# Performance work log

Hardware: AMD Instinct MI355X
Metric: run time of the kernel (lower is better)

## Reference

```python
import jax, jax.numpy as jnp
import numpy as np

B, TQ, TK, D, V = 16, 64, 512, 256, 32000


def setup_inputs() -> dict:
    key = jax.random.key(0)
    k = jax.random.split(key, 8)
    return {
        "domainslots": jax.random.normal(k[0], (B, TQ, D), jnp.float32),
        "out_states": jax.random.normal(k[1], (B, TQ, D), jnp.float32),
        "context": jax.random.normal(k[2], (B, TK, D), jnp.float32),
        "context_plain": jax.random.randint(k[3], (B, TK), 0, V, jnp.int64 if jax.config.jax_enable_x64 else jnp.int32),
        "W_state": jax.random.normal(k[4], (D, V), jnp.float32) * 0.02,
        "b_state": jnp.zeros((V,), jnp.float32),
        "W_gen": jax.random.normal(k[5], (3 * D, 1), jnp.float32) * 0.02,
        "b_gen": jnp.zeros((1,), jnp.float32),
    }


def reference(domainslots, out_states, context, context_plain, W_state, b_state, W_gen, b_gen):
    d = out_states.shape[-1]
    # pointer attention: softmax(Q K^T / sqrt(d)) over context  -> [B, TQ, TK]
    scores = jnp.einsum("bqd,bkd->bqk", out_states, context) / jnp.sqrt(jnp.asarray(d, out_states.dtype))
    pointer_attn = jax.nn.softmax(scores, axis=-1)

    # generation distribution over vocab  -> [B, TQ, V]
    p_state_vocab = jax.nn.softmax(out_states @ W_state + b_state, axis=-1)

    # copy distribution: scatter-add attention mass onto source token ids
    b_idx = jnp.arange(B)[:, None, None]           # [B,1,1]
    q_idx = jnp.arange(TQ)[None, :, None]          # [1,TQ,1]
    v_idx = context_plain[:, None, :]              # [B,1,TK] broadcast over TQ
    p_state_ptr = jnp.zeros((B, TQ, V), p_state_vocab.dtype).at[b_idx, q_idx, v_idx].add(pointer_attn)

    # attention-weighted context vector  -> [B, TQ, D]
    context_vec = jnp.einsum("bqk,bkd->bqd", pointer_attn, context)

    # generation gate  -> [B, TQ, 1]
    p_gen_vec = jnp.concatenate([out_states, context_vec, domainslots], axis=-1)
    p_state_gen = jax.nn.sigmoid(p_gen_vec @ W_gen + b_gen)

    p_state_out = p_state_gen * p_state_vocab + (1.0 - p_state_gen) * p_state_ptr
    return jnp.log(p_state_out)
```

## Files before the change

kernel.cpp:

```cpp
#include <hip/hip_runtime.h>
#include <math.h>

typedef short short8 __attribute__((ext_vector_type(8)));
typedef float f32x4 __attribute__((ext_vector_type(4)));

#define B_ 16
#define TQ_ 64
#define TK_ 512
#define D_ 256
#define V_ 32000
#define M_ (B_ * TQ_)

__device__ __forceinline__ unsigned short f2bf(float x) {
    unsigned int u = __float_as_uint(x);
    unsigned int r = (u + 0x7fffu + ((u >> 16) & 1u)) >> 16;
    return (unsigned short)r;
}

__device__ __forceinline__ void gload_lds16(const void* g, void* l) {
    __builtin_amdgcn_global_load_lds(
        (const __attribute__((address_space(1))) void*)g,
        (__attribute__((address_space(3))) void*)l, 16, 0, 0);
}

__global__ __launch_bounds__(256) void dedup_kernel(
    const int* __restrict__ cp, int* __restrict__ nexta, int* __restrict__ leader)
{
    __shared__ __align__(16) int c[TK_];
    const int b = blockIdx.x, tid = threadIdx.x;
    c[tid] = cp[b * TK_ + tid];
    c[tid + 256] = cp[b * TK_ + 256 + tid];
    __syncthreads();
    for (int k = tid; k < TK_; k += 256) {
        const int v = c[k];
        int fm = 1024, nx = 1024;
#pragma unroll 8
        for (int j0 = 0; j0 < TK_; j0 += 4) {
            const int4 q = *(const int4*)&c[j0];
            if (q.x == v) { fm = min(fm, j0);     if (j0     > k) nx = min(nx, j0);     }
            if (q.y == v) { fm = min(fm, j0 + 1); if (j0 + 1 > k) nx = min(nx, j0 + 1); }
            if (q.z == v) { fm = min(fm, j0 + 2); if (j0 + 2 > k) nx = min(nx, j0 + 2); }
            if (q.w == v) { fm = min(fm, j0 + 3); if (j0 + 3 > k) nx = min(nx, j0 + 3); }
        }
        nexta[b * TK_ + k] = (nx < 1024) ? nx : -1;
        leader[b * TK_ + k] = (fm == k) ? 1 : 0;
    }
}

__global__ __launch_bounds__(256) void conv_a_kernel(
    const float* __restrict__ A, unsigned short* __restrict__ Ab)
{
    const int i = (blockIdx.x * 256 + threadIdx.x) * 4;
    const float4 v = *(const float4*)&A[i];
    ushort4 o;
    o.x = f2bf(v.x); o.y = f2bf(v.y); o.z = f2bf(v.z); o.w = f2bf(v.w);
    *(ushort4*)&Ab[i] = o;
}

__global__ __launch_bounds__(256) void conv_w_kernel(
    const float* __restrict__ W, unsigned short* __restrict__ Wt)
{
    __shared__ float tile[64][65];
    const int tid = threadIdx.x;
    const int k0 = (blockIdx.x & 3) * 64;
    const int n0 = (blockIdx.x >> 2) * 64;
#pragma unroll
    for (int i = 0; i < 16; i++) {
        const int r = i * 4 + (tid >> 6), cc = tid & 63;
        tile[r][cc] = W[(k0 + r) * V_ + n0 + cc];
    }
    __syncthreads();
#pragma unroll
    for (int i = 0; i < 4; i++) {
        const int nl = i * 16 + (tid >> 4);
        const int kq = (tid & 15) * 4;
        ushort4 o;
        o.x = f2bf(tile[kq + 0][nl]);
        o.y = f2bf(tile[kq + 1][nl]);
        o.z = f2bf(tile[kq + 2][nl]);
        o.w = f2bf(tile[kq + 3][nl]);
        *(ushort4*)&Wt[(n0 + nl) * D_ + k0 + kq] = o;
    }
}

__global__ __launch_bounds__(256) void conv_c_kernel(
    const float* __restrict__ ctx, unsigned short* __restrict__ Cb,
    unsigned short* __restrict__ Ct)
{
    __shared__ float tile[64][65];
    const int tid = threadIdx.x;
    const int b = blockIdx.x >> 5;
    const int r5 = blockIdx.x & 31;
    const int k0 = (r5 >> 2) * 64;
    const int d0 = (r5 & 3) * 64;
#pragma unroll
    for (int i = 0; i < 16; i++) {
        const int r = i * 4 + (tid >> 6), cc = tid & 63;
        const float v = ctx[((b * TK_) + k0 + r) * D_ + d0 + cc];
        tile[r][cc] = v;
        Cb[((b * TK_) + k0 + r) * D_ + d0 + cc] = f2bf(v);
    }
    __syncthreads();
#pragma unroll
    for (int i = 0; i < 4; i++) {
        const int dl = i * 16 + (tid >> 4);
        const int kq = (tid & 15) * 4;
        ushort4 o;
        o.x = f2bf(tile[kq + 0][dl]);
        o.y = f2bf(tile[kq + 1][dl]);
        o.z = f2bf(tile[kq + 2][dl]);
        o.w = f2bf(tile[kq + 3][dl]);
        *(ushort4*)&Ct[((b * D_) + d0 + dl) * TK_ + k0 + kq] = o;
    }
}

template <int LDA, int LDB, int KTOT>
__global__ __launch_bounds__(256) void gemm_small(
    const unsigned short* __restrict__ A,
    const unsigned short* __restrict__ Bt,
    float* __restrict__ C, int ldc, int nchunks, int btrows, float scale)
{
    __shared__ short Al[64][72];
    __shared__ short Bl[128][72];
    const int tid = threadIdx.x;
    const int b = blockIdx.x / nchunks;
    const int n0 = (blockIdx.x % nchunks) * 128;
    A += (size_t)b * 64 * LDA;
    Bt += (size_t)b * btrows * LDB;
    C += (size_t)b * 64 * ldc;

    const int wid = tid >> 6;
    const int lane = tid & 63;
    const int wm = wid & 1, wn = wid >> 1;
    const int quad = lane >> 4, l15 = lane & 15;

    f32x4 acc[2][4];
#pragma unroll
    for (int i = 0; i < 2; i++)
#pragma unroll
        for (int j = 0; j < 4; j++) acc[i][j] = f32x4{0.f, 0.f, 0.f, 0.f};

    for (int k0 = 0; k0 < KTOT; k0 += 64) {
        __syncthreads();
#pragma unroll
        for (int i = 0; i < 2; i++) {
            const int c = tid + i * 256;
            const int r = c >> 3, kc = (c & 7) * 8;
            *(uint4*)&Al[r][kc] = *(const uint4*)&A[r * LDA + k0 + kc];
        }
#pragma unroll
        for (int i = 0; i < 4; i++) {
            const int c = tid + i * 256;
            const int r = c >> 3, kc = (c & 7) * 8;
            *(uint4*)&Bl[r][kc] = *(const uint4*)&Bt[(n0 + r) * LDB + k0 + kc];
        }
        __syncthreads();
#pragma unroll
        for (int ks = 0; ks < 64; ks += 32) {
            short8 af[2], bf[4];
#pragma unroll
            for (int mt = 0; mt < 2; mt++)
                af[mt] = *(const short8*)&Al[wm * 32 + mt * 16 + l15][ks + quad * 8];
#pragma unroll
            for (int nt = 0; nt < 4; nt++)
                bf[nt] = *(const short8*)&Bl[wn * 64 + nt * 16 + l15][ks + quad * 8];
#pragma unroll
            for (int mt = 0; mt < 2; mt++)
#pragma unroll
                for (int nt = 0; nt < 4; nt++)
                    acc[mt][nt] = __builtin_amdgcn_mfma_f32_16x16x32_bf16(
                        af[mt], bf[nt], acc[mt][nt], 0, 0, 0);
        }
    }
#pragma unroll
    for (int mt = 0; mt < 2; mt++)
#pragma unroll
        for (int nt = 0; nt < 4; nt++)
#pragma unroll
            for (int r = 0; r < 4; r++) {
                const int rl = wm * 32 + mt * 16 + quad * 4 + r;
                const int col = n0 + wn * 64 + nt * 16 + l15;
                C[rl * ldc + col] = acc[mt][nt][r] * scale;
            }
}

__global__ __launch_bounds__(256) void softmax_kernel(
    float* __restrict__ S, unsigned short* __restrict__ Pb)
{
    const int w = threadIdx.x >> 6, lane = threadIdx.x & 63;
    const int row = blockIdx.x * 4 + w;
    float v[8], m = -1e30f;
#pragma unroll
    for (int j = 0; j < 8; j++) { v[j] = S[row * TK_ + lane + 64 * j]; m = fmaxf(m, v[j]); }
#pragma unroll
    for (int off = 32; off; off >>= 1) m = fmaxf(m, __shfl_xor(m, off));
    float s = 0.f;
#pragma unroll
    for (int j = 0; j < 8; j++) { v[j] = __expf(v[j] - m); s += v[j]; }
#pragma unroll
    for (int off = 32; off; off >>= 1) s += __shfl_xor(s, off);
    const float inv = 1.0f / s;
#pragma unroll
    for (int j = 0; j < 8; j++) {
        const float p = v[j] * inv;
        S[row * TK_ + lane + 64 * j] = p;
        Pb[row * TK_ + lane + 64 * j] = f2bf(p);
    }
}

__global__ __launch_bounds__(256) void pgen_kernel(
    const float* __restrict__ os, const float* __restrict__ cv,
    const float* __restrict__ dm, const float* __restrict__ W_gen,
    const float* __restrict__ b_gen, float* __restrict__ pg)
{
    const int w = threadIdx.x >> 6, lane = threadIdx.x & 63;
    const int row = blockIdx.x * 4 + w;
    const int d4 = lane * 4;
    const float4 o4 = *(const float4*)&os[row * D_ + d4];
    const float4 c4 = *(const float4*)&cv[row * D_ + d4];
    const float4 m4 = *(const float4*)&dm[row * D_ + d4];
    const float4 w0 = *(const float4*)&W_gen[d4];
    const float4 w1 = *(const float4*)&W_gen[D_ + d4];
    const float4 w2 = *(const float4*)&W_gen[2 * D_ + d4];
    float p = o4.x * w0.x + o4.y * w0.y + o4.z * w0.z + o4.w * w0.w
            + c4.x * w1.x + c4.y * w1.y + c4.z * w1.z + c4.w * w1.w
            + m4.x * w2.x + m4.y * w2.y + m4.z * w2.z + m4.w * w2.w;
#pragma unroll
    for (int off = 32; off; off >>= 1) p += __shfl_xor(p, off);
    if (lane == 0) pg[row] = 1.0f / (1.0f + __expf(-(p + b_gen[0])));
}

__global__ __launch_bounds__(256) void gemm_vocab_fused(
    const unsigned short* __restrict__ A,
    const unsigned short* __restrict__ Bt,
    const float* __restrict__ b_state,
    float* __restrict__ Z,
    float* __restrict__ out)
{
    __shared__ short Al[128][64];
    __shared__ short Bl[128][64];
    __shared__ float bst[128];

    const int tid = threadIdx.x;
    const int bx = blockIdx.x;
    const int m0 = (bx & 7) * 128;
    const int n0 = (bx >> 3) * 128;

    if (tid < 128) bst[tid] = b_state[n0 + tid];

    const int wid = tid >> 6, lane = tid & 63;
    const int wm = wid & 1, wn = wid >> 1;
    const int quad = lane >> 4, l15 = lane & 15;
    const int srow = lane >> 3;
    const int scol = (lane & 7) * 8;

    f32x4 acc[4][4];
#pragma unroll
    for (int i = 0; i < 4; i++)
#pragma unroll
        for (int j = 0; j < 4; j++) acc[i][j] = f32x4{0.f, 0.f, 0.f, 0.f};

    for (int k0 = 0; k0 < D_; k0 += 64) {
        __syncthreads();
#pragma unroll
        for (int j = 0; j < 4; j++) {
            const int c = j * 4 + wid;
            const int r = c * 8 + srow;
            gload_lds16(&A[(size_t)(m0 + r) * D_ + k0 + scol], &Al[c * 8][0]);
        }
#pragma unroll
        for (int j = 0; j < 4; j++) {
            const int c = j * 4 + wid;
            const int r = c * 8 + srow;
            gload_lds16(&Bt[(size_t)(n0 + r) * D_ + k0 + scol], &Bl[c * 8][0]);
        }
        __syncthreads();
#pragma unroll
        for (int ks = 0; ks < 64; ks += 32) {
            short8 af[4], bf[4];
#pragma unroll
            for (int mt = 0; mt < 4; mt++)
                af[mt] = *(const short8*)&Al[wm * 64 + mt * 16 + l15][ks + quad * 8];
#pragma unroll
            for (int nt = 0; nt < 4; nt++)
                bf[nt] = *(const short8*)&Bl[wn * 64 + nt * 16 + l15][ks + quad * 8];
#pragma unroll
            for (int mt = 0; mt < 4; mt++)
#pragma unroll
                for (int nt = 0; nt < 4; nt++)
                    acc[mt][nt] = __builtin_amdgcn_mfma_f32_16x16x32_bf16(
                        af[mt], bf[nt], acc[mt][nt], 0, 0, 0);
        }
    }

#pragma unroll
    for (int mt = 0; mt < 4; mt++) {
        float rs[4] = {0.f, 0.f, 0.f, 0.f};
#pragma unroll
        for (int nt = 0; nt < 4; nt++) {
            const float bcol = bst[wn * 64 + nt * 16 + l15];
#pragma unroll
            for (int r = 0; r < 4; r++) {
                const int row = wm * 64 + mt * 16 + quad * 4 + r;
                const int col = wn * 64 + nt * 16 + l15;
                const float v = acc[mt][nt][r] + bcol;
                out[(size_t)(m0 + row) * V_ + n0 + col] = v;
                rs[r] += __expf(v);
            }
        }
#pragma unroll
        for (int r = 0; r < 4; r++) {
            float v = rs[r];
            v += __shfl_xor(v, 1);
            v += __shfl_xor(v, 2);
            v += __shfl_xor(v, 4);
            v += __shfl_xor(v, 8);
            if (l15 == 0)
                atomicAdd(&Z[m0 + wm * 64 + mt * 16 + quad * 4 + r], v);
        }
    }
}

__global__ __launch_bounds__(256) void rowconst_kernel(
    const float* __restrict__ pg, const float* __restrict__ Z, float* __restrict__ rc)
{
    const int r = blockIdx.x * 256 + threadIdx.x;
    rc[r] = logf(pg[r]) - logf(Z[r]);
}

__global__ __launch_bounds__(256) void epilogue_kernel(
    const float* __restrict__ rc, float* __restrict__ out)
{
    const int row = blockIdx.x;
    const float r = rc[row];
    float4* p = (float4*)(out + (size_t)row * V_);
    for (int i = threadIdx.x; i < V_ / 4; i += 256) {
        float4 v = p[i];
        v.x += r; v.y += r; v.z += r; v.w += r;
        p[i] = v;
    }
}

__global__ __launch_bounds__(256) void fixup_kernel(
    const int* __restrict__ cp, const int* __restrict__ nexta,
    const int* __restrict__ leader, const float* __restrict__ attn,
    const float* __restrict__ pg, float* __restrict__ out)
{
    const int t = blockIdx.x * 256 + threadIdx.x;
    const int row = t >> 9, k = t & 511;
    const int b = row >> 6;
    if (!leader[b * TK_ + k]) return;
    float a = attn[row * TK_ + k];
    int j = nexta[b * TK_ + k];
    while (j >= 0) { a += attn[row * TK_ + j]; j = nexta[b * TK_ + j]; }
    const float val = (1.0f - pg[row]) * a;
    const int v = cp[b * TK_ + k];
    const size_t idx = (size_t)row * V_ + v;
    out[idx] = logf(expf(out[idx]) + val);
}

extern "C" void kernel_launch(void* const* d_in, const int* in_sizes, int n_in,
                              void* d_out, int out_size, void* d_ws, size_t ws_size,
                              hipStream_t stream)
{
    const float* domainslots = (const float*)d_in[0];
    const float* out_states  = (const float*)d_in[1];
    const float* context     = (const float*)d_in[2];
    const int*   cp          = (const int*)d_in[3];
    const float* W_state     = (const float*)d_in[4];
    const float* b_state     = (const float*)d_in[5];
    const float* W_gen       = (const float*)d_in[6];
    const float* b_gen       = (const float*)d_in[7];
    float* out = (float*)d_out;
    char* ws = (char*)d_ws;

    float* Z      = (float*)(ws);
    float* pg     = (float*)(ws + 4096);
    float* rc     = (float*)(ws + 8192);
    float* S      = (float*)(ws + 12288);
    int* nexta    = (int*)(ws + 2109440);
    int* leader   = (int*)(ws + 2142208);
    unsigned short* Ab = (unsigned short*)(ws + 2174976);
    unsigned short* Wt = (unsigned short*)(ws + 2699264);
    unsigned short* Cb = (unsigned short*)(ws + 19083264);
    unsigned short* Ct = (unsigned short*)(ws + 23277568);
    unsigned short* Pb = (unsigned short*)(ws + 27471872);
    float* cv     = (float*)(ws + 28520448);

    hipMemsetAsync(Z, 0, M_ * sizeof(float), stream);
    dedup_kernel<<<B_, 256, 0, stream>>>(cp, nexta, leader);
    conv_a_kernel<<<(M_ * D_) / 1024, 256, 0, stream>>>(out_states, Ab);
    conv_w_kernel<<<(D_ / 64) * (V_ / 64), 256, 0, stream>>>(W_state, Wt);
    conv_c_kernel<<<B_ * 32, 256, 0, stream>>>(context, Cb, Ct);

    gemm_small<D_, D_, D_><<<B_ * 4, 256, 0, stream>>>(Ab, Cb, S, TK_, 4, TK_, 0.0625f);
    softmax_kernel<<<M_ / 4, 256, 0, stream>>>(S, Pb);
    gemm_small<TK_, TK_, TK_><<<B_ * 2, 256, 0, stream>>>(Pb, Ct, cv, D_, 2, D_, 1.0f);
    pgen_kernel<<<M_ / 4, 256, 0, stream>>>(out_states, cv, domainslots, W_gen, b_gen, pg);

    gemm_vocab_fused<<<(M_ / 128) * (V_ / 128), 256, 0, stream>>>(Ab, Wt, b_state, Z, out);
    rowconst_kernel<<<M_ / 256, 256, 0, stream>>>(pg, Z, rc);
    epilogue_kernel<<<M_, 256, 0, stream>>>(rc, out);
    fixup_kernel<<<(M_ * TK_) / 256, 256, 0, stream>>>(cp, nexta, leader, S, pg, out);
}
```

Measured before the change: 349.6 us.

## Recompute vocab GEMM twice to drop the logits read-modify-write epilogue

Splits the fused vocab GEMM into two passes. The first computes only the per-row exp-sums Z with no output store. The second recomputes the GEMM and writes the final log-probabilities directly, folding in log(pg) - log(Z) per row. This replaces the separate rowconst and epilogue kernels, removing a full read and write of the 131 MB output in exchange for doubling the bf16 GEMM work. Block indices are also swizzled across the grid so that concurrently running blocks share tiles differently for cache reuse.

```diff
diff --git a/kernel.cpp b/kernel.cpp
--- a/kernel.cpp
+++ b/kernel.cpp
@@ -230,21 +230,20 @@
     if (lane == 0) pg[row] = 1.0f / (1.0f + __expf(-(p + b_gen[0])));
 }
 
-__global__ __launch_bounds__(256) void gemm_vocab_fused(
+__global__ __launch_bounds__(256) void gemm_vocab_z(
     const unsigned short* __restrict__ A,
     const unsigned short* __restrict__ Bt,
     const float* __restrict__ b_state,
-    float* __restrict__ Z,
-    float* __restrict__ out)
+    float* __restrict__ Z)
 {
     __shared__ short Al[128][64];
     __shared__ short Bl[128][64];
     __shared__ float bst[128];
 
     const int tid = threadIdx.x;
-    const int bx = blockIdx.x;
-    const int m0 = (bx & 7) * 128;
-    const int n0 = (bx >> 3) * 128;
+    const int swz = (blockIdx.x & 7) * 250 + (blockIdx.x >> 3);
+    const int m0 = (swz & 7) * 128;
+    const int n0 = (swz >> 3) * 128;
 
     if (tid < 128) bst[tid] = b_state[n0 + tid];
 
@@ -300,13 +299,8 @@
         for (int nt = 0; nt < 4; nt++) {
             const float bcol = bst[wn * 64 + nt * 16 + l15];
 #pragma unroll
-            for (int r = 0; r < 4; r++) {
-                const int row = wm * 64 + mt * 16 + quad * 4 + r;
-                const int col = wn * 64 + nt * 16 + l15;
-                const float v = acc[mt][nt][r] + bcol;
-                out[(size_t)(m0 + row) * V_ + n0 + col] = v;
-                rs[r] += __expf(v);
-            }
+            for (int r = 0; r < 4; r++)
+                rs[r] += __expf(acc[mt][nt][r] + bcol);
         }
 #pragma unroll
         for (int r = 0; r < 4; r++) {
@@ -321,23 +315,86 @@
     }
 }
 
-__global__ __launch_bounds__(256) void rowconst_kernel(
-    const float* __restrict__ pg, const float* __restrict__ Z, float* __restrict__ rc)
-{
-    const int r = blockIdx.x * 256 + threadIdx.x;
-    rc[r] = logf(pg[r]) - logf(Z[r]);
-}
-
-__global__ __launch_bounds__(256) void epilogue_kernel(
-    const float* __restrict__ rc, float* __restrict__ out)
-{
-    const int row = blockIdx.x;
-    const float r = rc[row];
-    float4* p = (float4*)(out + (size_t)row * V_);
-    for (int i = threadIdx.x; i < V_ / 4; i += 256) {
-        float4 v = p[i];
-        v.x += r; v.y += r; v.z += r; v.w += r;
-        p[i] = v;
+__global__ __launch_bounds__(256) void gemm_vocab_out(
+    const unsigned short* __restrict__ A,
+    const unsigned short* __restrict__ Bt,
+    const float* __restrict__ b_state,
+    const float* __restrict__ pg,
+    const float* __restrict__ Z,
+    float* __restrict__ out)
+{
+    __shared__ short Al[128][64];
+    __shared__ short Bl[128][64];
+    __shared__ float bst[128];
+    __shared__ float rcs[128];
+
+    const int tid = threadIdx.x;
+    const int swz = (blockIdx.x & 7) * 250 + (blockIdx.x >> 3);
+    const int m0 = (swz & 7) * 128;
+    const int n0 = (swz >> 3) * 128;
+
+    if (tid < 128) {
+        bst[tid] = b_state[n0 + tid];
+        rcs[tid] = logf(pg[m0 + tid]) - logf(Z[m0 + tid]);
+    }
+
+    const int wid = tid >> 6, lane = tid & 63;
+    const int wm = wid & 1, wn = wid >> 1;
+    const int quad = lane >> 4, l15 = lane & 15;
+    const int srow = lane >> 3;
+    const int scol = (lane & 7) * 8;
+
+    f32x4 acc[4][4];
+#pragma unroll
+    for (int i = 0; i < 4; i++)
+#pragma unroll
+        for (int j = 0; j < 4; j++) acc[i][j] = f32x4{0.f, 0.f, 0.f, 0.f};
+
+    for (int k0 = 0; k0 < D_; k0 += 64) {
+        __syncthreads();
+#pragma unroll
+        for (int j = 0; j < 4; j++) {
+            const int c = j * 4 + wid;
+            const int r = c * 8 + srow;
+            gload_lds16(&A[(size_t)(m0 + r) * D_ + k0 + scol], &Al[c * 8][0]);
+        }
+#pragma unroll
+        for (int j = 0; j < 4; j++) {
+            const int c = j * 4 + wid;
+            const int r = c * 8 + srow;
+            gload_lds16(&Bt[(size_t)(n0 + r) * D_ + k0 + scol], &Bl[c * 8][0]);
+        }
+        __syncthreads();
+#pragma unroll
+        for (int ks = 0; ks < 64; ks += 32) {
+            short8 af[4], bf[4];
+#pragma unroll
+            for (int mt = 0; mt < 4; mt++)
+                af[mt] = *(const short8*)&Al[wm * 64 + mt * 16 + l15][ks + quad * 8];
+#pragma unroll
+            for (int nt = 0; nt < 4; nt++)
+                bf[nt] = *(const short8*)&Bl[wn * 64 + nt * 16 + l15][ks + quad * 8];
+#pragma unroll
+            for (int mt = 0; mt < 4; mt++)
+#pragma unroll
+                for (int nt = 0; nt < 4; nt++)
+                    acc[mt][nt] = __builtin_amdgcn_mfma_f32_16x16x32_bf16(
+                        af[mt], bf[nt], acc[mt][nt], 0, 0, 0);
+        }
+    }
+
+#pragma unroll
+    for (int mt = 0; mt < 4; mt++) {
+#pragma unroll
+        for (int nt = 0; nt < 4; nt++) {
+            const float bcol = bst[wn * 64 + nt * 16 + l15];
+#pragma unroll
+            for (int r = 0; r < 4; r++) {
+                const int row = wm * 64 + mt * 16 + quad * 4 + r;
+                const int col = wn * 64 + nt * 16 + l15;
+                out[(size_t)(m0 + row) * V_ + n0 + col] = acc[mt][nt][r] + bcol + rcs[row];
+            }
+        }
     }
 }
 
@@ -376,7 +433,6 @@
 
     float* Z      = (float*)(ws);
     float* pg     = (float*)(ws + 4096);
-    float* rc     = (float*)(ws + 8192);
     float* S      = (float*)(ws + 12288);
     int* nexta    = (int*)(ws + 2109440);
     int* leader   = (int*)(ws + 2142208);
@@ -398,8 +454,7 @@
     gemm_small<TK_, TK_, TK_><<<B_ * 2, 256, 0, stream>>>(Pb, Ct, cv, D_, 2, D_, 1.0f);
     pgen_kernel<<<M_ / 4, 256, 0, stream>>>(out_states, cv, domainslots, W_gen, b_gen, pg);
 
-    gemm_vocab_fused<<<(M_ / 128) * (V_ / 128), 256, 0, stream>>>(Ab, Wt, b_state, Z, out);
-    rowconst_kernel<<<M_ / 256, 256, 0, stream>>>(pg, Z, rc);
-    epilogue_kernel<<<M_, 256, 0, stream>>>(rc, out);
+    gemm_vocab_z<<<(M_ / 128) * (V_ / 128), 256, 0, stream>>>(Ab, Wt, b_state, Z);
+    gemm_vocab_out<<<(M_ / 128) * (V_ / 128), 256, 0, stream>>>(Ab, Wt, b_state, pg, Z, out);
     fixup_kernel<<<(M_ * TK_) / 256, 256, 0, stream>>>(cp, nexta, leader, S, pg, out);
 }
```

Measured after the change: 332.9 us. 1.05x faster.

## Recompute vocab GEMM in two passes to drop logits write and epilogue reread

Applied to the files above, without the earlier changes.

Splits the fused vocab GEMM into two passes. Pass one computes only the softmax row sums. Pass two recomputes the GEMM and writes the final log-probabilities with the row constant already added, which removes the separate epilogue kernel's read-modify-write over the 131 MB output. The GEMM now loads the full K=256 tile into XOR-swizzled LDS in one shot, with no k-loop syncs, and uses a block-index swizzle so blocks sharing the same W tile run together. The cost is doubled GEMM compute and 128 KB of LDS per block, which lowers occupancy.

```diff
diff --git a/kernel.cpp b/kernel.cpp
--- a/kernel.cpp
+++ b/kernel.cpp
@@ -230,29 +230,38 @@
     if (lane == 0) pg[row] = 1.0f / (1.0f + __expf(-(p + b_gen[0])));
 }
 
-__global__ __launch_bounds__(256) void gemm_vocab_fused(
+template <int PASS>
+__global__ __launch_bounds__(256) void gemm_vocab(
     const unsigned short* __restrict__ A,
     const unsigned short* __restrict__ Bt,
     const float* __restrict__ b_state,
+    const float* __restrict__ rc,
     float* __restrict__ Z,
     float* __restrict__ out)
 {
-    __shared__ short Al[128][64];
-    __shared__ short Bl[128][64];
-    __shared__ float bst[128];
+    __shared__ short Al[128][256];
+    __shared__ short Bl[128][256];
 
     const int tid = threadIdx.x;
-    const int bx = blockIdx.x;
-    const int m0 = (bx & 7) * 128;
-    const int n0 = (bx >> 3) * 128;
-
-    if (tid < 128) bst[tid] = b_state[n0 + tid];
+    const int swz = (blockIdx.x & 7) * 250 + (blockIdx.x >> 3);
+    const int m0 = (swz & 7) * 128;
+    const int n0 = (swz >> 3) * 128;
 
     const int wid = tid >> 6, lane = tid & 63;
     const int wm = wid & 1, wn = wid >> 1;
     const int quad = lane >> 4, l15 = lane & 15;
-    const int srow = lane >> 3;
-    const int scol = (lane & 7) * 8;
+
+    const int rpar = lane >> 5;
+    const int slot = lane & 31;
+#pragma unroll
+    for (int j = 0; j < 16; j++) {
+        const int c = j * 4 + wid;
+        const int r = c * 2 + rpar;
+        const int ksrc = ((slot ^ (r & 7)) << 3);
+        gload_lds16(&A[(size_t)(m0 + r) * D_ + ksrc], &Al[c * 2][0]);
+        gload_lds16(&Bt[(size_t)(n0 + r) * D_ + ksrc], &Bl[c * 2][0]);
+    }
+    __syncthreads();
 
     f32x4 acc[4][4];
 #pragma unroll
@@ -260,85 +269,78 @@
 #pragma unroll
         for (int j = 0; j < 4; j++) acc[i][j] = f32x4{0.f, 0.f, 0.f, 0.f};
 
-    for (int k0 = 0; k0 < D_; k0 += 64) {
-        __syncthreads();
-#pragma unroll
-        for (int j = 0; j < 4; j++) {
-            const int c = j * 4 + wid;
-            const int r = c * 8 + srow;
-            gload_lds16(&A[(size_t)(m0 + r) * D_ + k0 + scol], &Al[c * 8][0]);
-        }
-#pragma unroll
-        for (int j = 0; j < 4; j++) {
-            const int c = j * 4 + wid;
-            const int r = c * 8 + srow;
-            gload_lds16(&Bt[(size_t)(n0 + r) * D_ + k0 + scol], &Bl[c * 8][0]);
-        }
-        __syncthreads();
-#pragma unroll
-        for (int ks = 0; ks < 64; ks += 32) {
-            short8 af[4], bf[4];
-#pragma unroll
-            for (int mt = 0; mt < 4; mt++)
-                af[mt] = *(const short8*)&Al[wm * 64 + mt * 16 + l15][ks + quad * 8];
+#pragma unroll
+    for (int ks = 0; ks < D_; ks += 32) {
+        short8 af[4], bf[4];
+#pragma unroll
+        for (int mt = 0; mt < 4; mt++) {
+            const int row = wm * 64 + mt * 16 + l15;
+            af[mt] = *(const short8*)&Al[row][(ks + quad * 8) ^ ((l15 & 7) << 3)];
+        }
+#pragma unroll
+        for (int nt = 0; nt < 4; nt++) {
+            const int row = wn * 64 + nt * 16 + l15;
+            bf[nt] = *(const short8*)&Bl[row][(ks + quad * 8) ^ ((l15 & 7) << 3)];
+        }
+#pragma unroll
+        for (int mt = 0; mt < 4; mt++)
 #pragma unroll
             for (int nt = 0; nt < 4; nt++)
-                bf[nt] = *(const short8*)&Bl[wn * 64 + nt * 16 + l15][ks + quad * 8];
-#pragma unroll
-            for (int mt = 0; mt < 4; mt++)
-#pragma unroll
-                for (int nt = 0; nt < 4; nt++)
-                    acc[mt][nt] = __builtin_amdgcn_mfma_f32_16x16x32_bf16(
-                        af[mt], bf[nt], acc[mt][nt], 0, 0, 0);
-        }
-    }
-
-#pragma unroll
-    for (int mt = 0; mt < 4; mt++) {
-        float rs[4] = {0.f, 0.f, 0.f, 0.f};
-#pragma unroll
-        for (int nt = 0; nt < 4; nt++) {
-            const float bcol = bst[wn * 64 + nt * 16 + l15];
+                acc[mt][nt] = __builtin_amdgcn_mfma_f32_16x16x32_bf16(
+                    af[mt], bf[nt], acc[mt][nt], 0, 0, 0);
+    }
+
+    float bcol[4];
+#pragma unroll
+    for (int nt = 0; nt < 4; nt++)
+        bcol[nt] = b_state[n0 + wn * 64 + nt * 16 + l15];
+
+    if (PASS == 0) {
+#pragma unroll
+        for (int mt = 0; mt < 4; mt++) {
+            float rs[4] = {0.f, 0.f, 0.f, 0.f};
+#pragma unroll
+            for (int nt = 0; nt < 4; nt++)
+#pragma unroll
+                for (int r = 0; r < 4; r++)
+                    rs[r] += __expf(acc[mt][nt][r] + bcol[nt]);
 #pragma unroll
             for (int r = 0; r < 4; r++) {
-                const int row = wm * 64 + mt * 16 + quad * 4 + r;
-                const int col = wn * 64 + nt * 16 + l15;
-                const float v = acc[mt][nt][r] + bcol;
-                out[(size_t)(m0 + row) * V_ + n0 + col] = v;
-                rs[r] += __expf(v);
+                float v = rs[r];
+                v += __shfl_xor(v, 1);
+                v += __shfl_xor(v, 2);
+                v += __shfl_xor(v, 4);
+                v += __shfl_xor(v, 8);
+                if (l15 == 0)
+                    atomicAdd(&Z[m0 + wm * 64 + mt * 16 + quad * 4 + r], v);
             }
         }
-#pragma unroll
-        for (int r = 0; r < 4; r++) {
-            float v = rs[r];
-            v += __shfl_xor(v, 1);
-            v += __shfl_xor(v, 2);
-            v += __shfl_xor(v, 4);
-            v += __shfl_xor(v, 8);
-            if (l15 == 0)
-                atomicAdd(&Z[m0 + wm * 64 + mt * 16 + quad * 4 + r], v);
-        }
+    } else {
+        float rcv[4][4];
+#pragma unroll
+        for (int mt = 0; mt < 4; mt++)
+#pragma unroll
+            for (int r = 0; r < 4; r++)
+                rcv[mt][r] = rc[m0 + wm * 64 + mt * 16 + quad * 4 + r];
+#pragma unroll
+        for (int mt = 0; mt < 4; mt++)
+#pragma unroll
+            for (int nt = 0; nt < 4; nt++)
+#pragma unroll
+                for (int r = 0; r < 4; r++) {
+                    const int row = wm * 64 + mt * 16 + quad * 4 + r;
+                    const int col = wn * 64 + nt * 16 + l15;
+                    out[(size_t)(m0 + row) * V_ + n0 + col] =
+                        acc[mt][nt][r] + bcol[nt] + rcv[mt][r];
+                }
     }
 }
 
 __global__ __launch_bounds__(256) void rowconst_kernel(
-    const float* __restrict__ pg, const float* __restrict__ Z, float* __restrict__ rc)
+    const float* __restrict__ pg, const float* __restrict__ Z, float* __restrict__ rcv)
 {
     const int r = blockIdx.x * 256 + threadIdx.x;
-    rc[r] = logf(pg[r]) - logf(Z[r]);
-}
-
-__global__ __launch_bounds__(256) void epilogue_kernel(
-    const float* __restrict__ rc, float* __restrict__ out)
-{
-    const int row = blockIdx.x;
-    const float r = rc[row];
-    float4* p = (float4*)(out + (size_t)row * V_);
-    for (int i = threadIdx.x; i < V_ / 4; i += 256) {
-        float4 v = p[i];
-        v.x += r; v.y += r; v.z += r; v.w += r;
-        p[i] = v;
-    }
+    rcv[r] = logf(pg[r]) - logf(Z[r]);
 }
 
 __global__ __launch_bounds__(256) void fixup_kernel(
@@ -398,8 +400,8 @@
     gemm_small<TK_, TK_, TK_><<<B_ * 2, 256, 0, stream>>>(Pb, Ct, cv, D_, 2, D_, 1.0f);
     pgen_kernel<<<M_ / 4, 256, 0, stream>>>(out_states, cv, domainslots, W_gen, b_gen, pg);
 
-    gemm_vocab_fused<<<(M_ / 128) * (V_ / 128), 256, 0, stream>>>(Ab, Wt, b_state, Z, out);
+    gemm_vocab<0><<<(M_ / 128) * (V_ / 128), 256, 0, stream>>>(Ab, Wt, b_state, nullptr, Z, nullptr);
     rowconst_kernel<<<M_ / 256, 256, 0, stream>>>(pg, Z, rc);
-    epilogue_kernel<<<M_, 256, 0, stream>>>(rc, out);
+    gemm_vocab<1><<<(M_ / 128) * (V_ / 128), 256, 0, stream>>>(Ab, Wt, b_state, rc, nullptr, out);
     fixup_kernel<<<(M_ * TK_) / 256, 256, 0, stream>>>(cp, nexta, leader, S, pg, out);
 }
```

Result: faster. 342.2 us (-2.1%).
